# Optimization experiments

Hardware: AMD Instinct MI355X
Metric: run time of the kernel (lower is better)

The kernel has to match this reference:

```python
import jax, jax.numpy as jnp
import numpy as np

EMBED_DIM = 64   # conv out channels / linear in features
PATCH_DIM = 64   # linear out features
KSIZE, STRIDE, PAD = 5, 2, 2
B, T = 4, 480000


def setup_inputs() -> dict:
    key = jax.random.key(0)
    k1, k2, k3, k4, k5 = jax.random.split(key, 5)
    audio_waveform = jax.random.normal(k1, (B, T), jnp.float32)
    # conv1d weights: [out_ch, in_ch, k]
    conv_w = jax.random.normal(k2, (EMBED_DIM, 1, KSIZE), jnp.float32) / np.sqrt(KSIZE).astype(np.float32)
    conv_b = 0.01 * jax.random.normal(k3, (EMBED_DIM,), jnp.float32)
    # linear patch encoder: [patch_dim, embed_dim] (torch convention W @ x)
    lin_w = jax.random.normal(k4, (PATCH_DIM, EMBED_DIM), jnp.float32) / np.sqrt(EMBED_DIM).astype(np.float32)
    lin_b = 0.01 * jax.random.normal(k5, (PATCH_DIM,), jnp.float32)
    return dict(audio_waveform=audio_waveform, conv_w=conv_w, conv_b=conv_b,
                lin_w=lin_w, lin_b=lin_b)


def reference(audio_waveform, conv_w, conv_b, lin_w, lin_b):
    # [B, T] -> [B, 1, T]
    x = audio_waveform[:, None, :]
    # Conv1d(1 -> EMBED_DIM, k=5, stride=2, pad=2): [B, E, T//2]
    feats = jax.lax.conv_general_dilated(
        x, conv_w, window_strides=(STRIDE,), padding=[(PAD, PAD)],
        dimension_numbers=('NCH', 'OIH', 'NCH'))
    feats = jax.nn.relu(feats + conv_b[None, :, None])
    feats = feats.transpose(0, 2, 1)  # [B, seq_len, E]
    # Per-timestep linear patch encoder. NOTE: the torch module's
    # entropy-gated segmentation loop only chooses patch boundaries;
    # since patches are re-concatenated in order and the Linear is
    # applied per timestep, the output is exactly this, for any
    # entropy predictor / threshold.
    return jnp.einsum('bse,pe->bsp', feats, lin_w) + lin_b
```

## Files before the change

### kernel.cpp

```cpp
#include <hip/hip_runtime.h>
#include <hip/hip_bf16.h>
#include <stdint.h>

#define B_SZ    4
#define T_LEN   480000
#define S_LEN   240000
#define KS      5
#define PPB     7500
#define NPAIRS  (B_SZ * PPB)
#define GRID    512

static_assert(4 * GRID <= PPB, "single-wrap batch advance requires nw <= PPB");

typedef __attribute__((ext_vector_type(8))) __bf16  bf16x8;
typedef __attribute__((ext_vector_type(4))) float   f32x4;

__global__ __launch_bounds__(256) void audio_enc_kernel(
    const float* __restrict__ audio,
    const float* __restrict__ conv_w,
    const float* __restrict__ conv_b,
    const float* __restrict__ lin_w,
    const float* __restrict__ lin_b,
    float* __restrict__ out)
{
  const int lane = threadIdx.x & 63;
  const int m    = lane & 15;
  const int q    = lane >> 4;
  const int wid  = threadIdx.x >> 6;
  const int wv   = (int)((blockIdx.x << 2) | wid);
  const int nw   = (int)(gridDim.x << 2);

  __shared__ float lds[4][2048];
  float* const lw = lds[wid];

  float cw[2][8][KS], cbv[2][8];
#pragma unroll
  for (int h = 0; h < 2; ++h)
#pragma unroll
    for (int j = 0; j < 8; ++j) {
      const int e = h * 32 + q * 8 + j;
#pragma unroll
      for (int t = 0; t < KS; ++t) cw[h][j][t] = conv_w[e * KS + t];
      cbv[h][j] = conv_b[e];
    }

  bf16x8 wfrag[2][4];
#pragma unroll
  for (int nt = 0; nt < 4; ++nt) {
    const int p = nt * 16 + m;
#pragma unroll
    for (int kt = 0; kt < 2; ++kt) {
      const float* src = lin_w + p * 64 + kt * 32 + q * 8;
#pragma unroll
      for (int j = 0; j < 8; ++j) wfrag[kt][nt][j] = (__bf16)src[j];
    }
  }

  f32x4 lb4[4];
#pragma unroll
  for (int nt = 0; nt < 4; ++nt)
    lb4[nt] = *reinterpret_cast<const f32x4*>(lin_b + nt * 16 + q * 4);

  if (wv >= NPAIRS) return;
  int b0 = wv / PPB;
  int sp0 = wv - b0 * PPB;
  int sp1 = sp0 + nw, b1 = b0;
  if (sp1 >= PPB) { sp1 -= PPB; ++b1; }
  bool v1 = (b1 < B_SZ);

  auto load_tile = [&](int bb, int s0, float2& A, float2& Bv, float& C) {
    const float* base = audio + (size_t)bb * T_LEN;
    const int sl = s0 + m;
    const int gi = 2 * sl - 2;
    A = *reinterpret_cast<const float2*>(base + (gi < 0 ? 0 : gi));
    if (gi < 0) { A.x = 0.f; A.y = 0.f; }
    Bv = *reinterpret_cast<const float2*>(base + 2 * sl);
    const int ci = 2 * sl + 2;
    const float cv = base[ci < T_LEN ? ci : T_LEN - 1];
    C = (ci < T_LEN) ? cv : 0.f;
  };

  auto body = [&](const float* xs0, const float* xs1, int bc, int s0c) {
    bf16x8 xf0[2], xf1[2];
#pragma unroll
    for (int h = 0; h < 2; ++h)
#pragma unroll
      for (int j = 0; j < 8; ++j) {
        float a0 = cbv[h][j], a1 = cbv[h][j];
#pragma unroll
        for (int t = 0; t < KS; ++t) {
          a0 = fmaf(cw[h][j][t], xs0[t], a0);
          a1 = fmaf(cw[h][j][t], xs1[t], a1);
        }
        xf0[h][j] = (__bf16)fmaxf(a0, 0.f);
        xf1[h][j] = (__bf16)fmaxf(a1, 0.f);
      }

#pragma unroll
    for (int nt = 0; nt < 4; ++nt) {
      f32x4 acc0 = lb4[nt];
      acc0 = __builtin_amdgcn_mfma_f32_16x16x32_bf16(wfrag[0][nt], xf0[0], acc0, 0, 0, 0);
      acc0 = __builtin_amdgcn_mfma_f32_16x16x32_bf16(wfrag[1][nt], xf0[1], acc0, 0, 0, 0);
      *reinterpret_cast<f32x4*>(lw + m * 64 + ((nt * 16 + q * 4) ^ (m << 2))) = acc0;
      f32x4 acc1 = lb4[nt];
      acc1 = __builtin_amdgcn_mfma_f32_16x16x32_bf16(wfrag[0][nt], xf1[0], acc1, 0, 0, 0);
      acc1 = __builtin_amdgcn_mfma_f32_16x16x32_bf16(wfrag[1][nt], xf1[1], acc1, 0, 0, 0);
      *reinterpret_cast<f32x4*>(lw + 1024 + m * 64 + ((nt * 16 + q * 4) ^ (m << 2))) = acc1;
    }

    float* ob = out + ((size_t)bc * S_LEN + (size_t)s0c) * 64;
#pragma unroll
    for (int g = 0; g < 8; ++g) {
      const int r = (g & 3) * 4 + q;
      const f32x4 v = *reinterpret_cast<const f32x4*>(
          lw + (g >> 2) * 1024 + r * 64 + ((m << 2) ^ (r << 2)));
      *reinterpret_cast<f32x4*>(ob + g * 256 + lane * 4) = v;
    }
  };

  float2 A0a, B0a, A0b, B0b; float C0a, C0b;
  float2 A1a, B1a, A1b, B1b; float C1a, C1b;

  load_tile(b0, sp0 * 32,      A0a, B0a, C0a);
  load_tile(b0, sp0 * 32 + 16, A0b, B0b, C0b);
  if (v1) {
    load_tile(b1, sp1 * 32,      A1a, B1a, C1a);
    load_tile(b1, sp1 * 32 + 16, A1b, B1b, C1b);
  }

  while (true) {
    {
      const float xs0[KS] = {A0a.x, A0a.y, B0a.x, B0a.y, C0a};
      const float xs1[KS] = {A0b.x, A0b.y, B0b.x, B0b.y, C0b};
      int sp2 = sp1 + nw, b2 = b1;
      if (sp2 >= PPB) { sp2 -= PPB; ++b2; }
      const bool v2 = (b2 < B_SZ);
      if (v2) {
        load_tile(b2, sp2 * 32,      A0a, B0a, C0a);
        load_tile(b2, sp2 * 32 + 16, A0b, B0b, C0b);
      }
      body(xs0, xs1, b0, sp0 * 32);
      if (!v1) break;
      b0 = b1; sp0 = sp1; b1 = b2; sp1 = sp2; v1 = v2;
    }
    {
      const float xs0[KS] = {A1a.x, A1a.y, B1a.x, B1a.y, C1a};
      const float xs1[KS] = {A1b.x, A1b.y, B1b.x, B1b.y, C1b};
      int sp2 = sp1 + nw, b2 = b1;
      if (sp2 >= PPB) { sp2 -= PPB; ++b2; }
      const bool v2 = (b2 < B_SZ);
      if (v2) {
        load_tile(b2, sp2 * 32,      A1a, B1a, C1a);
        load_tile(b2, sp2 * 32 + 16, A1b, B1b, C1b);
      }
      body(xs0, xs1, b0, sp0 * 32);
      if (!v1) break;
      b0 = b1; sp0 = sp1; b1 = b2; sp1 = sp2; v1 = v2;
    }
  }
}

extern "C" void kernel_launch(void* const* d_in, const int* in_sizes, int n_in,
                              void* d_out, int out_size, void* d_ws, size_t ws_size,
                              hipStream_t stream) {
  const float* audio  = (const float*)d_in[0];
  const float* conv_w = (const float*)d_in[1];
  const float* conv_b = (const float*)d_in[2];
  const float* lin_w  = (const float*)d_in[3];
  const float* lin_b  = (const float*)d_in[4];
  float* out = (float*)d_out;

  audio_enc_kernel<<<dim3(GRID), dim3(256), 0, stream>>>(
      audio, conv_w, conv_b, lin_w, lin_b, out);
}
```

Measured before the change: 256.8 us.

## Pack conv weights as fp16 pairs, move linear bias to store path, enlarge grid

Conv weights and biases are held as packed fp16 pairs instead of fp32 registers, roughly halving their register footprint. The per-column linear bias is added once per output vector at store time instead of being held as four MFMA accumulator seeds. The grid grows from 512 to 768 blocks to use the freed registers for more resident waves. Rounding the conv weights to fp16 adds some precision loss, and converting fp16 back to float inside the loop adds ALU work.

```diff
diff --git a/kernel.cpp b/kernel.cpp
--- a/kernel.cpp
+++ b/kernel.cpp
@@ -8,12 +8,13 @@
 #define KS      5
 #define PPB     7500
 #define NPAIRS  (B_SZ * PPB)
-#define GRID    512
+#define GRID    768
 
 static_assert(4 * GRID <= PPB, "single-wrap batch advance requires nw <= PPB");
 
-typedef __attribute__((ext_vector_type(8))) __bf16  bf16x8;
-typedef __attribute__((ext_vector_type(4))) float   f32x4;
+typedef __attribute__((ext_vector_type(8))) __bf16    bf16x8;
+typedef __attribute__((ext_vector_type(4))) float     f32x4;
+typedef __attribute__((ext_vector_type(2))) _Float16  f16x2;
 
 __global__ __launch_bounds__(256) void audio_enc_kernel(
     const float* __restrict__ audio,
@@ -33,16 +34,24 @@
   __shared__ float lds[4][2048];
   float* const lw = lds[wid];
 
-  float cw[2][8][KS], cbv[2][8];
+  f16x2 cwp[2][8][3];
+  f16x2 cbp[2][4];
 #pragma unroll
-  for (int h = 0; h < 2; ++h)
+  for (int h = 0; h < 2; ++h) {
 #pragma unroll
     for (int j = 0; j < 8; ++j) {
       const int e = h * 32 + q * 8 + j;
+      const float* w = conv_w + e * KS;
+      cwp[h][j][0] = f16x2{(_Float16)w[0], (_Float16)w[1]};
+      cwp[h][j][1] = f16x2{(_Float16)w[2], (_Float16)w[3]};
+      cwp[h][j][2] = f16x2{(_Float16)w[4], (_Float16)0.f};
+    }
 #pragma unroll
-      for (int t = 0; t < KS; ++t) cw[h][j][t] = conv_w[e * KS + t];
-      cbv[h][j] = conv_b[e];
+    for (int jj = 0; jj < 4; ++jj) {
+      const int e = h * 32 + q * 8 + jj * 2;
+      cbp[h][jj] = f16x2{(_Float16)conv_b[e], (_Float16)conv_b[e + 1]};
     }
+  }
 
   bf16x8 wfrag[2][4];
 #pragma unroll
@@ -56,10 +65,7 @@
     }
   }
 
-  f32x4 lb4[4];
-#pragma unroll
-  for (int nt = 0; nt < 4; ++nt)
-    lb4[nt] = *reinterpret_cast<const f32x4*>(lin_b + nt * 16 + q * 4);
+  const f32x4 bias4 = *reinterpret_cast<const f32x4*>(lin_b + m * 4);
 
   if (wv >= NPAIRS) return;
   int b0 = wv / PPB;
@@ -86,23 +92,29 @@
     for (int h = 0; h < 2; ++h)
 #pragma unroll
       for (int j = 0; j < 8; ++j) {
-        float a0 = cbv[h][j], a1 = cbv[h][j];
-#pragma unroll
-        for (int t = 0; t < KS; ++t) {
-          a0 = fmaf(cw[h][j][t], xs0[t], a0);
-          a1 = fmaf(cw[h][j][t], xs1[t], a1);
-        }
+        const float w0 = (float)cwp[h][j][0][0];
+        const float w1 = (float)cwp[h][j][0][1];
+        const float w2 = (float)cwp[h][j][1][0];
+        const float w3 = (float)cwp[h][j][1][1];
+        const float w4 = (float)cwp[h][j][2][0];
+        const float bb = (float)cbp[h][j >> 1][j & 1];
+        float a0 = bb, a1 = bb;
+        a0 = fmaf(w0, xs0[0], a0);  a1 = fmaf(w0, xs1[0], a1);
+        a0 = fmaf(w1, xs0[1], a0);  a1 = fmaf(w1, xs1[1], a1);
+        a0 = fmaf(w2, xs0[2], a0);  a1 = fmaf(w2, xs1[2], a1);
+        a0 = fmaf(w3, xs0[3], a0);  a1 = fmaf(w3, xs1[3], a1);
+        a0 = fmaf(w4, xs0[4], a0);  a1 = fmaf(w4, xs1[4], a1);
         xf0[h][j] = (__bf16)fmaxf(a0, 0.f);
         xf1[h][j] = (__bf16)fmaxf(a1, 0.f);
       }
 
 #pragma unroll
     for (int nt = 0; nt < 4; ++nt) {
-      f32x4 acc0 = lb4[nt];
+      f32x4 acc0 = {0.f, 0.f, 0.f, 0.f};
       acc0 = __builtin_amdgcn_mfma_f32_16x16x32_bf16(wfrag[0][nt], xf0[0], acc0, 0, 0, 0);
       acc0 = __builtin_amdgcn_mfma_f32_16x16x32_bf16(wfrag[1][nt], xf0[1], acc0, 0, 0, 0);
       *reinterpret_cast<f32x4*>(lw + m * 64 + ((nt * 16 + q * 4) ^ (m << 2))) = acc0;
-      f32x4 acc1 = lb4[nt];
+      f32x4 acc1 = {0.f, 0.f, 0.f, 0.f};
       acc1 = __builtin_amdgcn_mfma_f32_16x16x32_bf16(wfrag[0][nt], xf1[0], acc1, 0, 0, 0);
       acc1 = __builtin_amdgcn_mfma_f32_16x16x32_bf16(wfrag[1][nt], xf1[1], acc1, 0, 0, 0);
       *reinterpret_cast<f32x4*>(lw + 1024 + m * 64 + ((nt * 16 + q * 4) ^ (m << 2))) = acc1;
@@ -112,8 +124,9 @@
 #pragma unroll
     for (int g = 0; g < 8; ++g) {
       const int r = (g & 3) * 4 + q;
-      const f32x4 v = *reinterpret_cast<const f32x4*>(
+      f32x4 v = *reinterpret_cast<const f32x4*>(
           lw + (g >> 2) * 1024 + r * 64 + ((m << 2) ^ (r << 2)));
+      v = v + bias4;
       *reinterpret_cast<f32x4*>(ob + g * 256 + lane * 4) = v;
     }
   };
```

Result: slower. 273.2 us (+6.4%).
